# Kernel tuning notes

Measured on AMD Instinct MI355X. Metric: run time of the kernel, lower is better.

Reference implementation:

```python
import jax, jax.numpy as jnp
import numpy as np

SIDES, LAYERS, NH = 2, 2, 2
DEPTH, B = 7, 8
NPT = (3 ** DEPTH - 1) // 2  # 1093 nodes per perfect ternary tree
N = B * NPT                  # 8744
E, H = 256, 512
NUM_USERS, NUM_POIS, NUM_CATS, NUM_COOS, TMAX = 2000, 5000, 300, 50, 600
FUSE = NUM_POIS + NUM_CATS + NUM_COOS


def setup_inputs() -> dict:
    key = jax.random.key(0)
    cnt = [0]
    def nk():
        cnt[0] += 1
        return jax.random.fold_in(key, cnt[0])
    def rn(*s):
        return jax.random.normal(nk(), s, jnp.float32) * 0.02
    inp = dict(
        user_ids=jax.random.randint(nk(), (SIDES, N), 0, NUM_USERS, jnp.int32),
        feat_ids=jax.random.randint(nk(), (SIDES, N), 0, FUSE, jnp.int32),
        time_ids=jax.random.randint(nk(), (SIDES, N), 0, TMAX, jnp.int32),
        mask=jnp.ones((SIDES, N), jnp.int32),
        depth=DEPTH, n_trees=B,
        user_emb=rn(SIDES, NUM_USERS, 128), fuse_emb=rn(SIDES, FUSE, 128),
        time_pe=rn(SIDES, TMAX, E),
        Wf=rn(SIDES, H, E), bf=jnp.zeros((SIDES, H)),
        Wiou=rn(SIDES, 3 * H, E), Uiou=rn(SIDES, 3 * H, 3 * H), biou=jnp.zeros((SIDES, 3 * H)),
        attn_in_w=rn(SIDES, LAYERS, 3 * H, H), attn_in_b=jnp.zeros((SIDES, LAYERS, 3 * H)),
        attn_out_w=rn(SIDES, LAYERS, H, H), attn_out_b=jnp.zeros((SIDES, LAYERS, H)),
        ff1_w=rn(SIDES, LAYERS, H, H), ff1_b=jnp.zeros((SIDES, LAYERS, H)),
        ff2_w=rn(SIDES, LAYERS, H, H), ff2_b=jnp.zeros((SIDES, LAYERS, H)),
        ln1_w=jnp.ones((SIDES, LAYERS, H)), ln1_b=jnp.zeros((SIDES, LAYERS, H)),
        ln2_w=jnp.ones((SIDES, LAYERS, H)), ln2_b=jnp.zeros((SIDES, LAYERS, H)),
        dec_poi_w=rn(SIDES, NUM_POIS, H), dec_poi_b=jnp.zeros((SIDES, NUM_POIS)),
        dec_cat_w=rn(SIDES, NUM_CATS, H), dec_cat_b=jnp.zeros((SIDES, NUM_CATS)),
        dec_coo_w=rn(SIDES, NUM_COOS, H), dec_coo_b=jnp.zeros((SIDES, NUM_COOS)),
        cat2poi_w=rn(SIDES, NUM_POIS, NUM_CATS), cat2poi_b=jnp.zeros((SIDES, NUM_POIS)),
        coo2poi_w=rn(SIDES, NUM_POIS, NUM_COOS), coo2poi_b=jnp.zeros((SIDES, NUM_POIS)),
        mtl=jnp.ones((SIDES, 3)),
        c0=(jax.random.uniform(nk(), (SIDES, N, H), jnp.float32) * 2.0 - 1.0) * 0.025,
    )
    return inp


def _ln(x, w, b, eps=1e-5):
    m = x.mean(-1, keepdims=True)
    v = ((x - m) ** 2).mean(-1, keepdims=True)
    return (x - m) / jnp.sqrt(v + eps) * w + b


def _mha(x, iw, ib, ow, ob):
    M, S, Hd = x.shape
    q, k, v = jnp.split(x @ iw.T + ib, 3, -1)
    hd = Hd // NH
    def rs(t):
        return t.reshape(M, S, NH, hd).transpose(0, 2, 1, 3)
    q, k, v = rs(q), rs(k), rs(v)
    att = jax.nn.softmax((q * (hd ** -0.5)) @ k.transpose(0, 1, 3, 2), -1)
    o = (att @ v).transpose(0, 2, 1, 3).reshape(M, S, Hd)
    return o @ ow.T + ob


def _enc(x, iw, ib, ow, ob, f1w, f1b, f2w, f2b, l1w, l1b, l2w, l2b):
    # post-norm TransformerEncoderLayer, relu, eval mode (no dropout)
    x = _ln(x + _mha(x, iw, ib, ow, ob), l1w, l1b)
    return _ln(x + (jax.nn.relu(x @ f1w.T + f1b) @ f2w.T + f2b), l2w, l2b)


def _forward(user_ids, feat_ids, time_ids, mask, depth, n_trees,
             user_emb, fuse_emb, time_pe, Wf, bf, Wiou, Uiou, biou,
             attn_in_w, attn_in_b, attn_out_w, attn_out_b,
             ff1_w, ff1_b, ff2_w, ff2_b, ln1_w, ln1_b, ln2_w, ln2_b,
             dec_poi_w, dec_poi_b, dec_cat_w, dec_cat_b, dec_coo_w, dec_coo_b,
             cat2poi_w, cat2poi_b, coo2poi_w, coo2poi_b, mtl, c0):
    Hd = Wf.shape[1]
    npt = (3 ** depth - 1) // 2
    Bt = n_trees
    offs = [(3 ** l - 1) // 2 for l in range(depth)]
    outs = []
    for s in range(SIDES):
        m = mask[s]
        uid, fid, tid = user_ids[s] * m, feat_ids[s] * m, time_ids[s] * m
        emb = jnp.concatenate([user_emb[s][uid], fuse_emb[s][fid]], -1) + 0.5 * time_pe[s][tid]
        mf = m.astype(emb.dtype)[:, None]
        x = (emb * mf).reshape(Bt, npt, -1)              # masked node features
        iou0 = ((emb @ Wiou[s].T) * mf).reshape(Bt, npt, 3 * Hd)  # leaf iou init
        c0s = c0[s].reshape(Bt, npt, Hd)
        h = jnp.zeros((Bt, npt, Hd), emb.dtype)
        c = jnp.zeros((Bt, npt, Hd), emb.dtype)
        for l in range(depth - 1, -1, -1):  # bottom-up topo propagation, level-major layout
            st, n = offs[l], 3 ** l
            if l == depth - 1:  # leaves: no reduce, apply with initial iou and c
                iou = iou0[:, st:st + n]
                cpre = c0s[:, st:st + n]
            else:
                cs = offs[l + 1]
                hch = h[:, cs:cs + 3 * n].reshape(Bt * n, 3, Hd)   # mailbox h_child
                cch = c[:, cs:cs + 3 * n].reshape(Bt, n, 3, Hd)    # mailbox c_child
                z = hch
                for L in range(LAYERS):
                    z = _enc(z, attn_in_w[s, L], attn_in_b[s, L], attn_out_w[s, L], attn_out_b[s, L],
                             ff1_w[s, L], ff1_b[s, L], ff2_w[s, L], ff2_b[s, L],
                             ln1_w[s, L], ln1_b[s, L], ln2_w[s, L], ln2_b[s, L])
                hc = z.reshape(Bt, n, 3 * Hd)
                xl = x[:, st:st + n]
                Wx = xl @ Wf[s].T
                f = jax.nn.sigmoid(jnp.concatenate([Wx] * 3, -1) + hc + jnp.tile(bf[s], 3))
                iou = xl @ Wiou[s].T + hc @ Uiou[s].T + biou[s]
                cpre = jnp.sum(f.reshape(Bt, n, 3, Hd) * cch, axis=2)
            i, o, u = jnp.split(iou, 3, -1)
            cn = jax.nn.sigmoid(i) * jnp.tanh(u) + cpre
            hn = jax.nn.sigmoid(o) * jnp.tanh(cn)
            h = h.at[:, st:st + n].set(hn)
            c = c.at[:, st:st + n].set(cn)
        hN = h.reshape(-1, Hd)
        poi = hN @ dec_poi_w[s].T + dec_poi_b[s]
        cat = hN @ dec_cat_w[s].T + dec_cat_b[s]
        coo = hN @ dec_coo_w[s].T + dec_coo_b[s]
        p = mtl[s]
        poi_mt = (0.5 * jnp.exp(-p[0]) * poi + p[0]
                  + 0.5 * jnp.exp(-p[1]) * (cat @ cat2poi_w[s].T + cat2poi_b[s]) + p[1]
                  + 0.5 * jnp.exp(-p[2]) * (coo @ coo2poi_w[s].T + coo2poi_b[s]) + p[2])
        outs += [poi_mt, cat, coo]
    return tuple(outs)


def reference(user_ids, feat_ids, time_ids, mask, depth, n_trees,
              user_emb, fuse_emb, time_pe, Wf, bf, Wiou, Uiou, biou,
              attn_in_w, attn_in_b, attn_out_w, attn_out_b,
              ff1_w, ff1_b, ff2_w, ff2_b, ln1_w, ln1_b, ln2_w, ln2_b,
              dec_poi_w, dec_poi_b, dec_cat_w, dec_cat_b, dec_coo_w, dec_coo_b,
              cat2poi_w, cat2poi_b, coo2poi_w, coo2poi_b, mtl, c0):
    return _forward(user_ids, feat_ids, time_ids, mask, depth, n_trees,
                    user_emb, fuse_emb, time_pe, Wf, bf, Wiou, Uiou, biou,
                    attn_in_w, attn_in_b, attn_out_w, attn_out_b,
                    ff1_w, ff1_b, ff2_w, ff2_b, ln1_w, ln1_b, ln2_w, ln2_b,
                    dec_poi_w, dec_poi_b, dec_cat_w, dec_cat_b, dec_coo_w, dec_coo_b,
                    cat2poi_w, cat2poi_b, coo2poi_w, coo2poi_b, mtl, c0)
```

## Files before the change

kernel.cpp:

```cpp
#include <hip/hip_runtime.h>
#include <math.h>

#define SIDES 2
#define LAYERS 2
#define NTREE 8
#define NPT 1093
#define NN (NTREE*NPT)
#define EE 256
#define HH 512
#define NUSERS 2000
#define NPOI 5000
#define NCAT 300
#define NCOO 50
#define FUSEN 5350
#define TMAXN 600
#define TOKMAX 5832
#define PARMAX 1944

constexpr long OUT_S   = 46780400L;
constexpr long CAT_OFF = 43720000L;
constexpr long COO_OFF = 46343200L;

constexpr long H_S    = (long)NN*HH;
constexpr long X_S    = (long)NN*EE;
constexpr long Z_S    = (long)TOKMAX*HH;
constexpr long QKV_S  = (long)TOKMAX*3*HH;
constexpr long WXI_S  = (long)PARMAX*2048;
constexpr long WEFF_S = (long)NPOI*HH;

typedef __attribute__((ext_vector_type(8))) short  bf16x8;
typedef __attribute__((ext_vector_type(8))) ushort u16x8;
typedef __attribute__((ext_vector_type(4))) ushort u16x4;
typedef __attribute__((ext_vector_type(4))) float  f32x4;

__device__ __forceinline__ float sigm(float x){ return 1.f/(1.f+expf(-x)); }
__device__ __forceinline__ ushort f2b(float f){
  union { float f; unsigned u; } v; v.f = f;
  return (ushort)((v.u + 0x7fffu + ((v.u >> 16) & 1u)) >> 16);
}
__device__ __forceinline__ float b2f(ushort u){
  union { unsigned u; float f; } v; v.u = (unsigned)u << 16; return v.f;
}

constexpr int PB_EMB  = 2*NN;
constexpr int PB_MCVT = 6494;
constexpr int PB_WCOMB= 2*2048;
constexpr int PB_BCOMB= 16;
constexpr int PB_POI  = 2*5000;
constexpr int PB_TP   = 2*512;
constexpr int PB_WEI  = 2*2500;
constexpr int PB_BEF  = 40;
constexpr int PB_TOT  = PB_EMB+PB_MCVT+PB_WCOMB+PB_BCOMB+PB_POI+PB_TP+PB_WEI+PB_BEF;

__global__ void __launch_bounds__(256) prep_k(
    const int* __restrict__ uid, const int* __restrict__ fid,
    const int* __restrict__ tids, const int* __restrict__ mask,
    const float* __restrict__ uemb, const float* __restrict__ femb,
    const float* __restrict__ tpe, ushort* __restrict__ X,
    ushort* ainW, const float* attn_in_w, ushort* aoutW, const float* attn_out_w,
    ushort* f1W, const float* ff1_w, ushort* f2W, const float* ff2_w,
    ushort* dcatW, const float* dec_cat_w, ushort* dcooW, const float* dec_coo_w,
    ushort* wcomb, const float* Wf, const float* Wiou, const float* Uiou,
    float* bcomb, const float* biou,
    ushort* c2pB, const float* cat2poi_w, ushort* o2pB, const float* coo2poi_w,
    ushort* dcT2,
    ushort* weffB, const float* dec_poi_w, const float* mtl,
    float* beff, const float* dec_poi_b, const float* dec_cat_b,
    const float* cat2poi_b, const float* dec_coo_b, const float* coo2poi_b){
  int b = blockIdx.x;
  int tid = threadIdx.x;
  if (b < PB_EMB){
    int s = b / NN; long i = b - s*NN; int d = tid;
    int m = mask[(long)s*NN + i];
    int u = uid[(long)s*NN + i]*m, f = fid[(long)s*NN + i]*m, t = tids[(long)s*NN + i]*m;
    float e = (d < 128) ? uemb[((long)s*NUSERS + u)*128 + d]
                        : femb[((long)s*FUSEN + f)*128 + (d-128)];
    e += 0.5f * tpe[((long)s*TMAXN + t)*256 + d];
    X[(long)s*X_S + i*EE + d] = f2b(e * (float)m);
    return;
  }
  b -= PB_EMB;
  if (b < PB_MCVT){
    const long n0 = 3145728, n1 = 1048576, n2 = 1048576, n3 = 1048576,
               n4 = 307200, n5 = 51200;
    long i = ((long)b*256 + tid)*4;
    ushort* d; const float* s; long off;
    if      (i < n0){ d=ainW;  s=attn_in_w;  off=i; }
    else if ((i-=n0) < n1){ d=aoutW; s=attn_out_w; off=i; }
    else if ((i-=n1) < n2){ d=f1W;  s=ff1_w;  off=i; }
    else if ((i-=n2) < n3){ d=f2W;  s=ff2_w;  off=i; }
    else if ((i-=n3) < n4){ d=dcatW; s=dec_cat_w; off=i; }
    else if ((i-=n4) < n5){ d=dcooW; s=dec_coo_w; off=i; }
    else return;
    f32x4 v = *(const f32x4*)(s + off);
    *(u16x4*)(d + off) = (u16x4){f2b(v[0]), f2b(v[1]), f2b(v[2]), f2b(v[3])};
    return;
  }
  b -= PB_MCVT;
  if (b < PB_WCOMB){
    int s = b >> 11; int row = b & 2047;
    ushort* dst = wcomb + (long)s*2048*1792 + (long)row*1792;
    for (int col = tid; col < 1792; col += 256){
      float v;
      if (row < 512) v = (col < 256) ? Wf[((long)s*512 + row)*256 + col] : 0.f;
      else {
        int r = row - 512;
        v = (col < 256) ? Wiou[((long)s*1536 + r)*256 + col]
                        : Uiou[((long)s*1536 + r)*1536 + (col-256)];
      }
      dst[col] = f2b(v);
    }
    return;
  }
  b -= PB_WCOMB;
  if (b < PB_BCOMB){
    int s = b >> 3; int c = (b & 7)*256 + tid;
    bcomb[(long)s*2048 + c] = (c < 512) ? 0.f : biou[(long)s*1536 + (c-512)];
    return;
  }
  b -= PB_BCOMB;
  if (b < PB_POI){
    int s = b / 5000; int r = b - s*5000;
    float a1 = 0.5f*expf(-mtl[(long)s*3 + 1]);
    float a2 = 0.5f*expf(-mtl[(long)s*3 + 2]);
    for (int c = tid; c < 320; c += 256){
      float v = (c < 300) ? a1*cat2poi_w[((long)s*5000 + r)*300 + c] : 0.f;
      c2pB[((long)s*5000 + r)*320 + c] = f2b(v);
    }
    if (tid < 64){
      float v = (tid < 50) ? a2*coo2poi_w[((long)s*5000 + r)*50 + tid] : 0.f;
      o2pB[((long)s*5000 + r)*64 + tid] = f2b(v);
    }
    return;
  }
  b -= PB_POI;
  if (b < PB_TP){
    int s = b >> 9; int h = b & 511;
    ushort* dst = dcT2 + ((long)s*512 + h)*384;
    for (int c = tid; c < 384; c += 256){
      float v = 0.f;
      if (c < 300)                  v = dec_cat_w[((long)s*300 + c)*512 + h];
      else if (c >= 320 && c < 370) v = dec_coo_w[((long)s*50 + (c-320))*512 + h];
      dst[c] = f2b(v);
    }
    return;
  }
  b -= PB_TP;
  if (b < PB_WEI){
    int s = b / 2500; int blk = b - s*2500;
    long i = ((long)blk*256 + tid)*4;
    float a0 = 0.5f*expf(-mtl[(long)s*3]);
    f32x4 v = *(const f32x4*)(dec_poi_w + (long)s*WEFF_S + i);
    *(u16x4*)(weffB + (long)s*WEFF_S + i) =
        (u16x4){f2b(a0*v[0]), f2b(a0*v[1]), f2b(a0*v[2]), f2b(a0*v[3])};
    return;
  }
  b -= PB_WEI;
  {
    int s = b / 20; int n = (b - s*20)*256 + tid;
    if (n >= NPOI) return;
    const float* mt = mtl + (long)s*3;
    float a0 = 0.5f*expf(-mt[0]), a1 = 0.5f*expf(-mt[1]), a2 = 0.5f*expf(-mt[2]);
    float acc1 = 0.f, acc2 = 0.f;
    for (int c = 0; c < NCAT; c++)
      acc1 += dec_cat_b[(long)s*NCAT + c] * cat2poi_w[((long)s*NPOI + n)*NCAT + c];
    for (int c = 0; c < NCOO; c++)
      acc2 += dec_coo_b[(long)s*NCOO + c] * coo2poi_w[((long)s*NPOI + n)*NCOO + c];
    beff[(long)s*NPOI + n] = a0*dec_poi_b[(long)s*NPOI + n]
        + a1*(acc1 + cat2poi_b[(long)s*NPOI + n]) + a2*(acc2 + coo2poi_b[(long)s*NPOI + n])
        + mt[0] + mt[1] + mt[2];
  }
}

template<int MODE, bool OBF>
__global__ void __launch_bounds__(256)
mgemm_k(const ushort* __restrict__ A1, long lda1, long sA1,
        const ushort* __restrict__ A2, long lda2, long sA2,
        int kSplit, int mapN, int mapOff,
        const ushort* __restrict__ Wt, long ldw, long sW,
        const float* __restrict__ bias, long sB,
        void* __restrict__ Cv, long ldc, long sC,
        int M, int Nc, int K, int nbx,
        const float* __restrict__ mtl, int mtlIdx){
  int s = blockIdx.z;
  A1 += (long)s*sA1; A2 += (long)s*sA2; Wt += (long)s*sW;
  if (bias) bias += (long)s*sB;

  int flat = blockIdx.x, nwg = gridDim.x;
  int xcd = flat & 7, q = nwg >> 3, r8 = nwg & 7;
  int nf = (xcd < r8 ? xcd*(q+1) : r8*(q+1) + (xcd - r8)*q) + (flat >> 3);
  int bx = nf % nbx, by = nf / nbx;
  int m0 = by*128, n0 = bx*128;

  __shared__ ushort As[128*64];
  __shared__ ushort Ws[128*64];

  int tid = threadIdx.x;
  int lane = tid & 63, wave = tid >> 6;
  int wr = wave >> 1, wc = wave & 1;
  int fr = lane & 15, kc = lane >> 4;

  int baseRow = tid >> 3;
  int c16 = tid & 7;
  int col8 = c16*8;
  int swz = (baseRow & 7) << 4;

  long gA1[4], gA2[4], gW[4];
  int wbyte[4];
  #pragma unroll
  for (int c = 0; c < 4; c++){
    int row = baseRow + c*32;
    int ra = m0 + row; if (ra > M-1) ra = M-1;
    gA2[c] = ra;
    if (mapN > 0){ int tr = ra / mapN; gA1[c] = (long)(tr*NPT + mapOff + (ra - tr*mapN)); }
    else gA1[c] = ra;
    int rw = n0 + row; if (rw > Nc-1) rw = Nc-1;
    gW[c] = rw;
    wbyte[c] = row*128 + ((c16*16) ^ swz);
  }

  u16x8 rA[4], rW[4];
  {
    bool u1 = (0 < kSplit);
    const ushort* asrc = u1 ? A1 : A2;
    long ld = u1 ? lda1 : lda2;
    const long* g = u1 ? gA1 : gA2;
    #pragma unroll
    for (int c = 0; c < 4; c++){
      rA[c] = *(const u16x8*)(asrc + g[c]*ld + col8);
      rW[c] = *(const u16x8*)(Wt + gW[c]*ldw + col8);
    }
  }

  f32x4 acc[4][4];
  #pragma unroll
  for (int i = 0; i < 4; i++)
    #pragma unroll
    for (int j = 0; j < 4; j++) acc[i][j] = (f32x4){0.f,0.f,0.f,0.f};

  for (int k0 = 0; k0 < K; k0 += 64){
    #pragma unroll
    for (int c = 0; c < 4; c++){
      *(u16x8*)((char*)As + wbyte[c]) = rA[c];
      *(u16x8*)((char*)Ws + wbyte[c]) = rW[c];
    }
    __syncthreads();
    int kn = k0 + 64;
    if (kn < K){
      bool u1 = (kn < kSplit);
      const ushort* asrc = u1 ? A1 : A2;
      long ld = u1 ? lda1 : lda2;
      const long* g = u1 ? gA1 : gA2;
      long colb = u1 ? (long)kn : (long)(kn - kSplit);
      #pragma unroll
      for (int c = 0; c < 4; c++){
        rA[c] = *(const u16x8*)(asrc + g[c]*ld + colb + col8);
        rW[c] = *(const u16x8*)(Wt + gW[c]*ldw + kn + col8);
      }
    }
    #pragma unroll
    for (int h = 0; h < 2; h++){
      bf16x8 af[4], bw[4];
      #pragma unroll
      for (int i = 0; i < 4; i++){
        int row = wr*64 + i*16 + fr;
        int byo = row*128 + ((h*64 + kc*16) ^ ((row & 7) << 4));
        af[i] = *(const bf16x8*)((const char*)As + byo);
      }
      #pragma unroll
      for (int j = 0; j < 4; j++){
        int row = wc*64 + j*16 + fr;
        int byo = row*128 + ((h*64 + kc*16) ^ ((row & 7) << 4));
        bw[j] = *(const bf16x8*)((const char*)Ws + byo);
      }
      #pragma unroll
      for (int i = 0; i < 4; i++)
        #pragma unroll
        for (int j = 0; j < 4; j++)
          acc[i][j] = __builtin_amdgcn_mfma_f32_16x16x32_bf16(bw[j], af[i], acc[i][j], 0, 0, 0);
    }
    __syncthreads();
  }

  float alpha = 1.f;
  if (MODE == 4) alpha = 0.5f*expf(-mtl[(long)s*3 + mtlIdx]);
  int ccol = lane & 15, cr4 = (lane >> 4)*4;
  bool vecN = ((Nc & 3) == 0);
  float* Cf = (float*)Cv + (long)s*sC;
  ushort* Cb = (ushort*)Cv + (long)s*sC;
  #pragma unroll
  for (int i = 0; i < 4; i++){
    int gm = m0 + wr*64 + i*16 + ccol;
    if (gm >= M) continue;
    long rowoff = (long)gm*ldc;
    #pragma unroll
    for (int j = 0; j < 4; j++){
      int gn0 = n0 + wc*64 + j*16 + cr4;
      if (gn0 >= Nc) continue;
      f32x4 v = acc[i][j];
      if (MODE != 4 && MODE != 2 && bias){ f32x4 bv = *(const f32x4*)&bias[gn0]; v += bv; }
      if (MODE == 1){ v = (f32x4){fmaxf(v[0],0.f),fmaxf(v[1],0.f),fmaxf(v[2],0.f),fmaxf(v[3],0.f)}; }
      if (OBF){
        u16x4* cp = (u16x4*)&Cb[rowoff + gn0];
        if (MODE == 4 || MODE == 2){
          u16x4 o = *cp;
          float a = (MODE == 4) ? alpha : 1.f;
          *cp = (u16x4){f2b(b2f(o[0]) + a*v[0]), f2b(b2f(o[1]) + a*v[1]),
                        f2b(b2f(o[2]) + a*v[2]), f2b(b2f(o[3]) + a*v[3])};
        } else {
          *cp = (u16x4){f2b(v[0]), f2b(v[1]), f2b(v[2]), f2b(v[3])};
        }
      } else {
        if (vecN){
          f32x4* cp = (f32x4*)&Cf[rowoff + gn0];
          if (MODE == 4){ f32x4 o = *cp; *cp = o + alpha*v; }
          else if (MODE == 2){ f32x4 o = *cp; *cp = o + v; }
          else *cp = v;
        } else {
          #pragma unroll
          for (int r = 0; r < 4; r++){
            int gn = gn0 + r; if (gn >= Nc) continue;
            if (MODE == 4) Cf[rowoff + gn] += alpha*v[r];
            else if (MODE == 2) Cf[rowoff + gn] += v[r];
            else Cf[rowoff + gn] = v[r];
          }
        }
      }
    }
  }
}

__global__ void __launch_bounds__(256) attn_k(const ushort* __restrict__ qkv,
                                              ushort* __restrict__ o){
  int s = blockIdx.z;
  int w = threadIdx.x >> 6, lane = threadIdx.x & 63;
  int seq = blockIdx.x*2 + (w >> 1);
  int h = w & 1;
  const ushort* base = qkv + (long)s*QKV_S + (long)seq*3*1536 + h*256 + lane*4;
  float q[3][4], k[3][4], v[3][4];
  #pragma unroll
  for (int i = 0; i < 3; i++){
    u16x4 tq = *(const u16x4*)(base + (long)i*1536);
    u16x4 tk = *(const u16x4*)(base + (long)i*1536 + 512);
    u16x4 tv = *(const u16x4*)(base + (long)i*1536 + 1024);
    #pragma unroll
    for (int e = 0; e < 4; e++){ q[i][e]=b2f(tq[e]); k[i][e]=b2f(tk[e]); v[i][e]=b2f(tv[e]); }
  }
  float p[9];
  #pragma unroll
  for (int i = 0; i < 3; i++)
    #pragma unroll
    for (int j = 0; j < 3; j++){
      float acc = 0.f;
      #pragma unroll
      for (int e = 0; e < 4; e++) acc += q[i][e]*k[j][e];
      p[i*3+j] = acc;
    }
  #pragma unroll
  for (int m = 1; m < 64; m <<= 1)
    #pragma unroll
    for (int t = 0; t < 9; t++) p[t] += __shfl_xor(p[t], m);
  float att[9];
  #pragma unroll
  for (int i = 0; i < 3; i++){
    float a = p[i*3]*0.0625f, bb = p[i*3+1]*0.0625f, c = p[i*3+2]*0.0625f;
    float mx = fmaxf(a, fmaxf(bb, c));
    a = expf(a-mx); bb = expf(bb-mx); c = expf(c-mx);
    float inv = 1.f/(a+bb+c);
    att[i*3] = a*inv; att[i*3+1] = bb*inv; att[i*3+2] = c*inv;
  }
  ushort* ob = o + (long)s*Z_S + (long)seq*1536 + h*256 + lane*4;
  #pragma unroll
  for (int i = 0; i < 3; i++){
    u16x4 r;
    #pragma unroll
    for (int e = 0; e < 4; e++)
      r[e] = f2b(att[i*3]*v[0][e] + att[i*3+1]*v[1][e] + att[i*3+2]*v[2][e]);
    *(u16x4*)(ob + (long)i*512) = r;
  }
}

__global__ void __launch_bounds__(256) add_ln_k(ushort* __restrict__ zout, long sZ,
                         const ushort* __restrict__ res, long sR, int mapN, int mapOff,
                         const ushort* __restrict__ tb, long sT,
                         const float* __restrict__ w, const float* __restrict__ b,
                         long wstr){
  int s = blockIdx.z;
  int wv = threadIdx.x >> 6, lane = threadIdx.x & 63;
  int r = blockIdx.x*4 + wv;
  int g = r;
  if (mapN > 0){ int tr = r / mapN; g = tr*NPT + mapOff + (r - tr*mapN); }
  int d0 = lane*8;
  u16x8 rr = *(const u16x8*)(res + (long)s*sR + (long)g*HH + d0);
  u16x8 tt = *(const u16x8*)(tb  + (long)s*sT + (long)r*HH + d0);
  float x[8];
  float sum = 0.f;
  #pragma unroll
  for (int e = 0; e < 8; e++){ x[e] = b2f(rr[e]) + b2f(tt[e]); sum += x[e]; }
  #pragma unroll
  for (int m = 1; m < 64; m <<= 1) sum += __shfl_xor(sum, m);
  float mean = sum * (1.f/512.f);
  float vs = 0.f;
  #pragma unroll
  for (int e = 0; e < 8; e++){ float d = x[e]-mean; vs += d*d; }
  #pragma unroll
  for (int m = 1; m < 64; m <<= 1) vs += __shfl_xor(vs, m);
  float inv = 1.f/sqrtf(vs*(1.f/512.f) + 1e-5f);
  const float* wr_ = w + (long)s*wstr + d0;
  const float* br_ = b + (long)s*wstr + d0;
  f32x4 w0 = *(const f32x4*)wr_, w1 = *(const f32x4*)(wr_+4);
  f32x4 b0 = *(const f32x4*)br_, b1 = *(const f32x4*)(br_+4);
  u16x8 ov;
  #pragma unroll
  for (int e = 0; e < 4; e++){
    ov[e]   = f2b((x[e]-mean)*inv*w0[e] + b0[e]);
    ov[e+4] = f2b((x[e+4]-mean)*inv*w1[e] + b1[e]);
  }
  *(u16x8*)(zout + (long)s*sZ + (long)r*HH + d0) = ov;
}

__global__ void leaf_k(const ushort* __restrict__ iou, const float* __restrict__ c0,
                       ushort* __restrict__ hbuf, float* __restrict__ cbuf){
  int s = blockIdx.z, p = blockIdx.x;
  int tree = p / 729, j = p - tree*729;
  long row = (long)(tree*NPT + 364 + j)*HH;
  const ushort* iour = iou + (long)s*QKV_S + (long)p*1536;
  const float* c0r = c0 + (long)s*H_S + row;
  for (int d = threadIdx.x; d < HH; d += 256){
    float cn = sigm(b2f(iour[d])) * tanhf(b2f(iour[1024 + d])) + c0r[d];
    float hn = sigm(b2f(iour[512 + d])) * tanhf(cn);
    hbuf[(long)s*H_S + row + d] = f2b(hn);
    cbuf[(long)s*H_S + row + d] = cn;
  }
}

__global__ void combine_k(const ushort* __restrict__ wxiou, const ushort* __restrict__ z,
                          const float* __restrict__ bfv, const float* __restrict__ cbuf,
                          ushort* __restrict__ hbuf, float* __restrict__ cout,
                          int n, int st, int cs){
  int s = blockIdx.z, p = blockIdx.x;
  int tree = p / n, j = p - tree*n;
  const ushort* wr_ = wxiou + (long)s*WXI_S + (long)p*2048;
  const ushort* zr  = z + (long)s*Z_S + (long)p*1536;
  const float* bfr  = bfv + (long)s*HH;
  const float* cch  = cbuf + (long)s*H_S + (long)(tree*NPT + cs + 3*j)*HH;
  long orow = (long)s*H_S + (long)(tree*NPT + st + j)*HH;
  for (int d = threadIdx.x; d < HH; d += 256){
    float wv = b2f(wr_[d]) + bfr[d];
    float cpre = 0.f;
    #pragma unroll
    for (int ch = 0; ch < 3; ch++){
      float fg = sigm(wv + b2f(zr[ch*512 + d]));
      cpre += fg * cch[ch*512 + d];
    }
    float iv = b2f(wr_[512 + d]), ov = b2f(wr_[1024 + d]), uv = b2f(wr_[1536 + d]);
    float cn = sigm(iv)*tanhf(uv) + cpre;
    float hn = sigm(ov)*tanhf(cn);
    hbuf[orow + d] = f2b(hn);
    cout[orow + d] = cn;
  }
}

#define GEMM(MODE, OBF, A1, LDA1, SA1, A2, LDA2, SA2, KSPL, MAPN, MAPOFF, WT, LDW, SW, \
             BI, SB, CC, LDC, SC, M, NC, K)                                            \
  do { int nbx_ = ((NC)+127)/128, nby_ = ((M)+127)/128;                                \
    mgemm_k<MODE, OBF><<<dim3(nbx_*nby_, 1, SIDES), 256, 0, stream>>>(                 \
      A1, LDA1, SA1, A2, LDA2, SA2, KSPL, MAPN, MAPOFF, WT, LDW, SW, BI, SB,           \
      CC, LDC, SC, M, NC, K, nbx_, mtl, 0); } while(0)

extern "C" void kernel_launch(void* const* d_in, const int* in_sizes, int n_in,
                              void* d_out, int out_size, void* d_ws, size_t ws_size,
                              hipStream_t stream){
  (void)in_sizes; (void)n_in; (void)out_size; (void)ws_size;
  const int*   user_ids  = (const int*)d_in[0];
  const int*   feat_ids  = (const int*)d_in[1];
  const int*   time_ids  = (const int*)d_in[2];
  const int*   mask      = (const int*)d_in[3];
  const float* user_emb  = (const float*)d_in[6];
  const float* fuse_emb  = (const float*)d_in[7];
  const float* time_pe   = (const float*)d_in[8];
  const float* Wf        = (const float*)d_in[9];
  const float* bf        = (const float*)d_in[10];
  const float* Wiou      = (const float*)d_in[11];
  const float* Uiou      = (const float*)d_in[12];
  const float* biou      = (const float*)d_in[13];
  const float* attn_in_w = (const float*)d_in[14];
  const float* attn_in_b = (const float*)d_in[15];
  const float* attn_out_w= (const float*)d_in[16];
  const float* attn_out_b= (const float*)d_in[17];
  const float* ff1_w     = (const float*)d_in[18];
  const float* ff1_b     = (const float*)d_in[19];
  const float* ff2_w     = (const float*)d_in[20];
  const float* ff2_b     = (const float*)d_in[21];
  const float* ln1_w     = (const float*)d_in[22];
  const float* ln1_b     = (const float*)d_in[23];
  const float* ln2_w     = (const float*)d_in[24];
  const float* ln2_b     = (const float*)d_in[25];
  const float* dec_poi_w = (const float*)d_in[26];
  const float* dec_poi_b = (const float*)d_in[27];
  const float* dec_cat_w = (const float*)d_in[28];
  const float* dec_cat_b = (const float*)d_in[29];
  const float* dec_coo_w = (const float*)d_in[30];
  const float* dec_coo_b = (const float*)d_in[31];
  const float* cat2poi_w = (const float*)d_in[32];
  const float* cat2poi_b = (const float*)d_in[33];
  const float* coo2poi_w = (const float*)d_in[34];
  const float* coo2poi_b = (const float*)d_in[35];
  const float* mtl       = (const float*)d_in[36];
  const float* c0        = (const float*)d_in[37];

  float* out = (float*)d_out;

  ushort* wsu = (ushort*)d_ws;
  ushort* Hb    = wsu;
  ushort* ainW  = Hb    + 2*H_S;
  ushort* aoutW = ainW  + (long)2*2*1536*512;
  ushort* f1W   = aoutW + (long)2*2*512*512;
  ushort* f2W   = f1W   + (long)2*2*512*512;
  ushort* wcomb = f2W   + (long)2*2*512*512;
  ushort* dcatW = wcomb + (long)2*2048*1792;
  ushort* dcooW = dcatW + (long)2*300*512;
  ushort* weffB = dcooW + (long)2*50*512;
  float*  bcomb = (float*)(weffB + (long)2*WEFF_S);
  float*  beff  = bcomb + 2*2048;

  float*  Cb   = out + OUT_S;
  ushort* osu  = (ushort*)(Cb + 2*H_S);
  ushort* QKV  = osu;
  ushort* Zb   = QKV  + 2*QKV_S;
  ushort* TMP  = Zb   + 2*Z_S;
  ushort* WXI  = TMP  + 2*Z_S;
  ushort* Xb   = WXI  + 2*WXI_S;
  ushort* c2pB = Xb   + 2*X_S;
  ushort* o2pB = c2pB + (long)2*5000*320;
  ushort* dcT2 = o2pB + (long)2*5000*64;

  prep_k<<<dim3(PB_TOT), 256, 0, stream>>>(
      user_ids, feat_ids, time_ids, mask, user_emb, fuse_emb, time_pe, Xb,
      ainW, attn_in_w, aoutW, attn_out_w, f1W, ff1_w, f2W, ff2_w,
      dcatW, dec_cat_w, dcooW, dec_coo_w,
      wcomb, Wf, Wiou, Uiou, bcomb, biou,
      c2pB, cat2poi_w, o2pB, coo2poi_w, dcT2,
      weffB, dec_poi_w, mtl,
      beff, dec_poi_b, dec_cat_b, cat2poi_b, dec_coo_b, coo2poi_b);

  GEMM(0, true, Xb, 256L, X_S, Xb, 256L, X_S, 256, 729, 364,
       wcomb + (long)512*1792, 1792L, (long)2048*1792,
       (const float*)nullptr, 0L, QKV, 1536L, QKV_S, 5832, 1536, 256);
  leaf_k<<<dim3(5832, 1, SIDES), 256, 0, stream>>>(QKV, c0, Hb, Cb);

  const int p3[7]   = {1,3,9,27,81,243,729};
  const int offs[7] = {0,1,4,13,40,121,364};

  for (int l = 5; l >= 0; l--){
    int n = p3[l], st = offs[l], cs = offs[l+1];
    int P = NTREE*n, T = 3*P;
    for (int L = 0; L < LAYERS; L++){
      const ushort* zin = (L == 0) ? Hb : Zb;
      long zs = (L == 0) ? H_S : Z_S;
      int mN = (L == 0) ? 3*n : 0, mO = (L == 0) ? cs : 0;
      GEMM(0, true, zin, 512L, zs, zin, 512L, zs, 512, mN, mO,
           ainW + (long)L*1536*512, 512L, (long)2*1536*512,
           attn_in_b + (long)L*1536, (long)LAYERS*1536, QKV, 1536L, QKV_S, T, 1536, 512);
      attn_k<<<dim3(P/2, 1, SIDES), 256, 0, stream>>>(QKV, TMP);
      GEMM(0, true, TMP, 512L, Z_S, TMP, 512L, Z_S, 512, 0, 0,
           aoutW + (long)L*512*512, 512L, (long)2*512*512,
           attn_out_b + (long)L*512, (long)LAYERS*512, QKV, 512L, QKV_S, T, 512, 512);
      add_ln_k<<<dim3(T/4, 1, SIDES), 256, 0, stream>>>(Zb, Z_S, zin, zs, mN, mO,
           QKV, QKV_S, ln1_w + (long)L*512, ln1_b + (long)L*512, (long)LAYERS*512);
      GEMM(1, true, Zb, 512L, Z_S, Zb, 512L, Z_S, 512, 0, 0,
           f1W + (long)L*512*512, 512L, (long)2*512*512,
           ff1_b + (long)L*512, (long)LAYERS*512, TMP, 512L, Z_S, T, 512, 512);
      GEMM(0, true, TMP, 512L, Z_S, TMP, 512L, Z_S, 512, 0, 0,
           f2W + (long)L*512*512, 512L, (long)2*512*512,
           ff2_b + (long)L*512, (long)LAYERS*512, QKV, 512L, QKV_S, T, 512, 512);
      add_ln_k<<<dim3(T/4, 1, SIDES), 256, 0, stream>>>(Zb, Z_S, Zb, Z_S, 0, 0,
           QKV, QKV_S, ln2_w + (long)L*512, ln2_b + (long)L*512, (long)LAYERS*512);
    }
    GEMM(0, true, Xb, 256L, X_S, Zb, 1536L, Z_S, 256, n, st,
         wcomb, 1792L, (long)2048*1792, bcomb, 2048L, WXI, 2048L, WXI_S, P, 2048, 1792);
    combine_k<<<dim3(P, 1, SIDES), 256, 0, stream>>>(WXI, Zb, bf, Cb, Hb, Cb, n, st, cs);
  }

  GEMM(0, false, Hb, 512L, H_S, Hb, 512L, H_S, 512, 0, 0,
       dcatW, 512L, (long)NCAT*512, dec_cat_b, (long)NCAT,
       out + CAT_OFF, (long)NCAT, OUT_S, NN, NCAT, 512);
  GEMM(0, false, Hb, 512L, H_S, Hb, 512L, H_S, 512, 0, 0,
       dcooW, 512L, (long)NCOO*512, dec_coo_b, (long)NCOO,
       out + COO_OFF, (long)NCOO, OUT_S, NN, NCOO, 512);

  GEMM(2, true, c2pB, 320L, (long)5000*320, o2pB, 64L, (long)5000*64, 320, 0, 0,
       dcT2, 384L, (long)512*384, (const float*)nullptr, 0L,
       weffB, 512L, WEFF_S, 5000, 512, 384);

  GEMM(0, false, Hb, 512L, H_S, Hb, 512L, H_S, 512, 0, 0,
       weffB, 512L, WEFF_S, beff, (long)NPOI,
       out, (long)NPOI, OUT_S, NN, NPOI, 512);
}
```

Baseline: 1.554 ms.

## Fuse 3-token attention into the attention-output GEMM prologue

Removes the standalone attention kernel. Each GEMM block now computes the QK scores and softmax for its row range into shared memory, then builds the attention output on the fly while staging the A tile from the V columns. This drops one launch and the write and read of the intermediate attention buffer. In exchange, each of the 4 column blocks recomputes the scores, every A-tile load now reads three V rows with fp32 math in the load path, and the output goes to TMP instead of QKV.

```diff
diff --git a/kernel.cpp b/kernel.cpp
--- a/kernel.cpp
+++ b/kernel.cpp
@@ -172,7 +172,7 @@
   }
 }
 
-template<int MODE, bool OBF>
+template<int MODE, bool OBF, bool FATTN>
 __global__ void __launch_bounds__(256)
 mgemm_k(const ushort* __restrict__ A1, long lda1, long sA1,
         const ushort* __restrict__ A2, long lda2, long sA2,
@@ -194,6 +194,7 @@
 
   __shared__ ushort As[128*64];
   __shared__ ushort Ws[128*64];
+  __shared__ float satt[FATTN ? 792 : 1];
 
   int tid = threadIdx.x;
   int lane = tid & 63, wave = tid >> 6;
@@ -219,16 +220,76 @@
     wbyte[c] = row*128 + ((c16*16) ^ swz);
   }
 
+  int s0q = 0;
+  if constexpr (FATTN){
+    s0q = m0/3;
+    int lastRow = m0 + 127; if (lastRow > M-1) lastRow = M-1;
+    int nseq = lastRow/3 - s0q + 1;
+    for (int task = tid; task < nseq*18; task += 256){
+      int sl = task/18, rem = task - sl*18;
+      int h = rem/9, ij = rem - h*9;
+      int i2 = ij/3, j2 = ij - i2*3;
+      const ushort* qp = A1 + ((long)((s0q+sl)*3 + i2))*lda1 + h*256;
+      const ushort* kp = A1 + ((long)((s0q+sl)*3 + j2))*lda1 + 512 + h*256;
+      float accd = 0.f;
+      for (int c = 0; c < 256; c += 8){
+        u16x8 qv = *(const u16x8*)(qp + c);
+        u16x8 kv = *(const u16x8*)(kp + c);
+        #pragma unroll
+        for (int e = 0; e < 8; e++) accd += b2f(qv[e])*b2f(kv[e]);
+      }
+      satt[task] = accd * 0.0625f;
+    }
+    __syncthreads();
+    for (int task = tid; task < nseq*6; task += 256){
+      int sl = task/6, rem = task - sl*6;
+      int h = rem/3, i2 = rem - h*3;
+      float* p = &satt[sl*18 + h*9 + i2*3];
+      float a = p[0], bq = p[1], cq = p[2];
+      float mx = fmaxf(a, fmaxf(bq, cq));
+      a = expf(a-mx); bq = expf(bq-mx); cq = expf(cq-mx);
+      float inv = 1.f/(a+bq+cq);
+      p[0] = a*inv; p[1] = bq*inv; p[2] = cq*inv;
+    }
+    __syncthreads();
+  }
+
+  auto stageA = [&](int c, long kb) -> u16x8 {
+    int ra = (int)gA1[c];
+    int seq = ra/3, tok = ra - seq*3, sl = seq - s0q;
+    long d = kb + col8;
+    int h = (int)(d >> 8);
+    const float* at = &satt[sl*18 + h*9 + tok*3];
+    const ushort* vb = A1 + ((long)seq*3)*lda1 + 1024 + d;
+    u16x8 v0 = *(const u16x8*)(vb);
+    u16x8 v1 = *(const u16x8*)(vb + lda1);
+    u16x8 v2 = *(const u16x8*)(vb + 2*lda1);
+    float a0 = at[0], a1 = at[1], a2 = at[2];
+    u16x8 r;
+    #pragma unroll
+    for (int e = 0; e < 8; e++)
+      r[e] = f2b(a0*b2f(v0[e]) + a1*b2f(v1[e]) + a2*b2f(v2[e]));
+    return r;
+  };
+
   u16x8 rA[4], rW[4];
   {
-    bool u1 = (0 < kSplit);
-    const ushort* asrc = u1 ? A1 : A2;
-    long ld = u1 ? lda1 : lda2;
-    const long* g = u1 ? gA1 : gA2;
-    #pragma unroll
-    for (int c = 0; c < 4; c++){
-      rA[c] = *(const u16x8*)(asrc + g[c]*ld + col8);
-      rW[c] = *(const u16x8*)(Wt + gW[c]*ldw + col8);
+    if constexpr (FATTN){
+      #pragma unroll
+      for (int c = 0; c < 4; c++){
+        rA[c] = stageA(c, 0);
+        rW[c] = *(const u16x8*)(Wt + gW[c]*ldw + col8);
+      }
+    } else {
+      bool u1 = (0 < kSplit);
+      const ushort* asrc = u1 ? A1 : A2;
+      long ld = u1 ? lda1 : lda2;
+      const long* g = u1 ? gA1 : gA2;
+      #pragma unroll
+      for (int c = 0; c < 4; c++){
+        rA[c] = *(const u16x8*)(asrc + g[c]*ld + col8);
+        rW[c] = *(const u16x8*)(Wt + gW[c]*ldw + col8);
+      }
     }
   }
 
@@ -247,15 +308,23 @@
     __syncthreads();
     int kn = k0 + 64;
     if (kn < K){
-      bool u1 = (kn < kSplit);
-      const ushort* asrc = u1 ? A1 : A2;
-      long ld = u1 ? lda1 : lda2;
-      const long* g = u1 ? gA1 : gA2;
-      long colb = u1 ? (long)kn : (long)(kn - kSplit);
-      #pragma unroll
-      for (int c = 0; c < 4; c++){
-        rA[c] = *(const u16x8*)(asrc + g[c]*ld + colb + col8);
-        rW[c] = *(const u16x8*)(Wt + gW[c]*ldw + kn + col8);
+      if constexpr (FATTN){
+        #pragma unroll
+        for (int c = 0; c < 4; c++){
+          rA[c] = stageA(c, kn);
+          rW[c] = *(const u16x8*)(Wt + gW[c]*ldw + kn + col8);
+        }
+      } else {
+        bool u1 = (kn < kSplit);
+        const ushort* asrc = u1 ? A1 : A2;
+        long ld = u1 ? lda1 : lda2;
+        const long* g = u1 ? gA1 : gA2;
+        long colb = u1 ? (long)kn : (long)(kn - kSplit);
+        #pragma unroll
+        for (int c = 0; c < 4; c++){
+          rA[c] = *(const u16x8*)(asrc + g[c]*ld + colb + col8);
+          rW[c] = *(const u16x8*)(Wt + gW[c]*ldw + kn + col8);
+        }
       }
     }
     #pragma unroll
@@ -330,56 +399,6 @@
   }
 }
 
-__global__ void __launch_bounds__(256) attn_k(const ushort* __restrict__ qkv,
-                                              ushort* __restrict__ o){
-  int s = blockIdx.z;
-  int w = threadIdx.x >> 6, lane = threadIdx.x & 63;
-  int seq = blockIdx.x*2 + (w >> 1);
-  int h = w & 1;
-  const ushort* base = qkv + (long)s*QKV_S + (long)seq*3*1536 + h*256 + lane*4;
-  float q[3][4], k[3][4], v[3][4];
-  #pragma unroll
-  for (int i = 0; i < 3; i++){
-    u16x4 tq = *(const u16x4*)(base + (long)i*1536);
-    u16x4 tk = *(const u16x4*)(base + (long)i*1536 + 512);
-    u16x4 tv = *(const u16x4*)(base + (long)i*1536 + 1024);
-    #pragma unroll
-    for (int e = 0; e < 4; e++){ q[i][e]=b2f(tq[e]); k[i][e]=b2f(tk[e]); v[i][e]=b2f(tv[e]); }
-  }
-  float p[9];
-  #pragma unroll
-  for (int i = 0; i < 3; i++)
-    #pragma unroll
-    for (int j = 0; j < 3; j++){
-      float acc = 0.f;
-      #pragma unroll
-      for (int e = 0; e < 4; e++) acc += q[i][e]*k[j][e];
-      p[i*3+j] = acc;
-    }
-  #pragma unroll
-  for (int m = 1; m < 64; m <<= 1)
-    #pragma unroll
-    for (int t = 0; t < 9; t++) p[t] += __shfl_xor(p[t], m);
-  float att[9];
-  #pragma unroll
-  for (int i = 0; i < 3; i++){
-    float a = p[i*3]*0.0625f, bb = p[i*3+1]*0.0625f, c = p[i*3+2]*0.0625f;
-    float mx = fmaxf(a, fmaxf(bb, c));
-    a = expf(a-mx); bb = expf(bb-mx); c = expf(c-mx);
-    float inv = 1.f/(a+bb+c);
-    att[i*3] = a*inv; att[i*3+1] = bb*inv; att[i*3+2] = c*inv;
-  }
-  ushort* ob = o + (long)s*Z_S + (long)seq*1536 + h*256 + lane*4;
-  #pragma unroll
-  for (int i = 0; i < 3; i++){
-    u16x4 r;
-    #pragma unroll
-    for (int e = 0; e < 4; e++)
-      r[e] = f2b(att[i*3]*v[0][e] + att[i*3+1]*v[1][e] + att[i*3+2]*v[2][e]);
-    *(u16x4*)(ob + (long)i*512) = r;
-  }
-}
-
 __global__ void __launch_bounds__(256) add_ln_k(ushort* __restrict__ zout, long sZ,
                          const ushort* __restrict__ res, long sR, int mapN, int mapOff,
                          const ushort* __restrict__ tb, long sT,
@@ -464,9 +483,14 @@
 #define GEMM(MODE, OBF, A1, LDA1, SA1, A2, LDA2, SA2, KSPL, MAPN, MAPOFF, WT, LDW, SW, \
              BI, SB, CC, LDC, SC, M, NC, K)                                            \
   do { int nbx_ = ((NC)+127)/128, nby_ = ((M)+127)/128;                                \
-    mgemm_k<MODE, OBF><<<dim3(nbx_*nby_, 1, SIDES), 256, 0, stream>>>(                 \
+    mgemm_k<MODE, OBF, false><<<dim3(nbx_*nby_, 1, SIDES), 256, 0, stream>>>(          \
       A1, LDA1, SA1, A2, LDA2, SA2, KSPL, MAPN, MAPOFF, WT, LDW, SW, BI, SB,           \
       CC, LDC, SC, M, NC, K, nbx_, mtl, 0); } while(0)
+#define GEMMFA(QKVP, WT, LDW, SW, BI, SB, CC, LDC, SC, M)                              \
+  do { int nbx_ = 4, nby_ = ((M)+127)/128;                                            \
+    mgemm_k<0, true, true><<<dim3(nbx_*nby_, 1, SIDES), 256, 0, stream>>>(             \
+      QKVP, 1536L, QKV_S, QKVP, 1536L, QKV_S, 512, 0, 0, WT, LDW, SW, BI, SB,          \
+      CC, LDC, SC, M, 512, 512, nbx_, mtl, 0); } while(0)
 
 extern "C" void kernel_launch(void* const* d_in, const int* in_sizes, int n_in,
                               void* d_out, int out_size, void* d_ws, size_t ws_size,
@@ -562,12 +586,10 @@
       GEMM(0, true, zin, 512L, zs, zin, 512L, zs, 512, mN, mO,
            ainW + (long)L*1536*512, 512L, (long)2*1536*512,
            attn_in_b + (long)L*1536, (long)LAYERS*1536, QKV, 1536L, QKV_S, T, 1536, 512);
-      attn_k<<<dim3(P/2, 1, SIDES), 256, 0, stream>>>(QKV, TMP);
-      GEMM(0, true, TMP, 512L, Z_S, TMP, 512L, Z_S, 512, 0, 0,
-           aoutW + (long)L*512*512, 512L, (long)2*512*512,
-           attn_out_b + (long)L*512, (long)LAYERS*512, QKV, 512L, QKV_S, T, 512, 512);
+      GEMMFA(QKV, aoutW + (long)L*512*512, 512L, (long)2*512*512,
+             attn_out_b + (long)L*512, (long)LAYERS*512, TMP, 512L, Z_S, T);
       add_ln_k<<<dim3(T/4, 1, SIDES), 256, 0, stream>>>(Zb, Z_S, zin, zs, mN, mO,
-           QKV, QKV_S, ln1_w + (long)L*512, ln1_b + (long)L*512, (long)LAYERS*512);
+           TMP, Z_S, ln1_w + (long)L*512, ln1_b + (long)L*512, (long)LAYERS*512);
       GEMM(1, true, Zb, 512L, Z_S, Zb, 512L, Z_S, 512, 0, 0,
            f1W + (long)L*512*512, 512L, (long)2*512*512,
            ff1_b + (long)L*512, (long)LAYERS*512, TMP, 512L, Z_S, T, 512, 512);
```

After: 1.777 ms. +14.3%, slower.

## Widen GEMM tile to 128x256 with each wave owning a 64-column strip

Applied to the files above, without the earlier changes.

The GEMM block tile grows from 128x128 to 128x256 along N. The wave layout changes so each of the four waves covers all 128 rows and its own 64-column slice, which doubles the accumulators per wave to 8x4 MFMA tiles. The aim is more reuse of the A tile and fewer blocks, at the cost of more registers, twice the W shared memory, and fewer blocks for small-N GEMMs. A launch bound of 2 blocks per CU is added to limit register growth.

```diff
diff --git a/kernel.cpp b/kernel.cpp
--- a/kernel.cpp
+++ b/kernel.cpp
@@ -173,7 +173,7 @@
 }
 
 template<int MODE, bool OBF>
-__global__ void __launch_bounds__(256)
+__global__ void __launch_bounds__(256, 2)
 mgemm_k(const ushort* __restrict__ A1, long lda1, long sA1,
         const ushort* __restrict__ A2, long lda2, long sA2,
         int kSplit, int mapN, int mapOff,
@@ -190,23 +190,21 @@
   int xcd = flat & 7, q = nwg >> 3, r8 = nwg & 7;
   int nf = (xcd < r8 ? xcd*(q+1) : r8*(q+1) + (xcd - r8)*q) + (flat >> 3);
   int bx = nf % nbx, by = nf / nbx;
-  int m0 = by*128, n0 = bx*128;
+  int m0 = by*128, n0 = bx*256;
 
   __shared__ ushort As[128*64];
-  __shared__ ushort Ws[128*64];
+  __shared__ ushort Ws[256*64];
 
   int tid = threadIdx.x;
   int lane = tid & 63, wave = tid >> 6;
-  int wr = wave >> 1, wc = wave & 1;
   int fr = lane & 15, kc = lane >> 4;
 
   int baseRow = tid >> 3;
   int c16 = tid & 7;
   int col8 = c16*8;
-  int swz = (baseRow & 7) << 4;
-
-  long gA1[4], gA2[4], gW[4];
-  int wbyte[4];
+
+  long gA1[4], gA2[4], gW[8];
+  int abyte[4], wbyte[8];
   #pragma unroll
   for (int c = 0; c < 4; c++){
     int row = baseRow + c*32;
@@ -214,36 +212,43 @@
     gA2[c] = ra;
     if (mapN > 0){ int tr = ra / mapN; gA1[c] = (long)(tr*NPT + mapOff + (ra - tr*mapN)); }
     else gA1[c] = ra;
+    abyte[c] = row*128 + ((c16*16) ^ ((row & 7) << 4));
+  }
+  #pragma unroll
+  for (int c = 0; c < 8; c++){
+    int row = baseRow + c*32;
     int rw = n0 + row; if (rw > Nc-1) rw = Nc-1;
     gW[c] = rw;
-    wbyte[c] = row*128 + ((c16*16) ^ swz);
-  }
-
-  u16x8 rA[4], rW[4];
+    wbyte[c] = row*128 + ((c16*16) ^ ((row & 7) << 4));
+  }
+
+  u16x8 rA[4], rW[8];
   {
     bool u1 = (0 < kSplit);
     const ushort* asrc = u1 ? A1 : A2;
     long ld = u1 ? lda1 : lda2;
     const long* g = u1 ? gA1 : gA2;
     #pragma unroll
-    for (int c = 0; c < 4; c++){
+    for (int c = 0; c < 4; c++)
       rA[c] = *(const u16x8*)(asrc + g[c]*ld + col8);
+    #pragma unroll
+    for (int c = 0; c < 8; c++)
       rW[c] = *(const u16x8*)(Wt + gW[c]*ldw + col8);
-    }
-  }
-
-  f32x4 acc[4][4];
-  #pragma unroll
-  for (int i = 0; i < 4; i++)
+  }
+
+  f32x4 acc[8][4];
+  #pragma unroll
+  for (int i = 0; i < 8; i++)
     #pragma unroll
     for (int j = 0; j < 4; j++) acc[i][j] = (f32x4){0.f,0.f,0.f,0.f};
 
   for (int k0 = 0; k0 < K; k0 += 64){
     #pragma unroll
-    for (int c = 0; c < 4; c++){
-      *(u16x8*)((char*)As + wbyte[c]) = rA[c];
+    for (int c = 0; c < 4; c++)
+      *(u16x8*)((char*)As + abyte[c]) = rA[c];
+    #pragma unroll
+    for (int c = 0; c < 8; c++)
       *(u16x8*)((char*)Ws + wbyte[c]) = rW[c];
-    }
     __syncthreads();
     int kn = k0 + 64;
     if (kn < K){
@@ -251,33 +256,32 @@
       const ushort* asrc = u1 ? A1 : A2;
       long ld = u1 ? lda1 : lda2;
       const long* g = u1 ? gA1 : gA2;
-      long colb = u1 ? (long)kn : (long)(kn - kSplit);
+      long colb = (u1 ? (long)kn : (long)(kn - kSplit)) + col8;
       #pragma unroll
-      for (int c = 0; c < 4; c++){
-        rA[c] = *(const u16x8*)(asrc + g[c]*ld + colb + col8);
+      for (int c = 0; c < 4; c++)
+        rA[c] = *(const u16x8*)(asrc + g[c]*ld + colb);
+      #pragma unroll
+      for (int c = 0; c < 8; c++)
         rW[c] = *(const u16x8*)(Wt + gW[c]*ldw + kn + col8);
-      }
     }
     #pragma unroll
     for (int h = 0; h < 2; h++){
-      bf16x8 af[4], bw[4];
-      #pragma unroll
-      for (int i = 0; i < 4; i++){
-        int row = wr*64 + i*16 + fr;
-        int byo = row*128 + ((h*64 + kc*16) ^ ((row & 7) << 4));
-        af[i] = *(const bf16x8*)((const char*)As + byo);
-      }
+      bf16x8 bw[4];
       #pragma unroll
       for (int j = 0; j < 4; j++){
-        int row = wc*64 + j*16 + fr;
+        int row = wave*64 + j*16 + fr;
         int byo = row*128 + ((h*64 + kc*16) ^ ((row & 7) << 4));
         bw[j] = *(const bf16x8*)((const char*)Ws + byo);
       }
       #pragma unroll
-      for (int i = 0; i < 4; i++)
+      for (int i = 0; i < 8; i++){
+        int row = i*16 + fr;
+        int byo = row*128 + ((h*64 + kc*16) ^ ((row & 7) << 4));
+        bf16x8 af = *(const bf16x8*)((const char*)As + byo);
         #pragma unroll
         for (int j = 0; j < 4; j++)
-          acc[i][j] = __builtin_amdgcn_mfma_f32_16x16x32_bf16(bw[j], af[i], acc[i][j], 0, 0, 0);
+          acc[i][j] = __builtin_amdgcn_mfma_f32_16x16x32_bf16(bw[j], af, acc[i][j], 0, 0, 0);
+      }
     }
     __syncthreads();
   }
@@ -289,13 +293,13 @@
   float* Cf = (float*)Cv + (long)s*sC;
   ushort* Cb = (ushort*)Cv + (long)s*sC;
   #pragma unroll
-  for (int i = 0; i < 4; i++){
-    int gm = m0 + wr*64 + i*16 + ccol;
+  for (int i = 0; i < 8; i++){
+    int gm = m0 + i*16 + ccol;
     if (gm >= M) continue;
     long rowoff = (long)gm*ldc;
     #pragma unroll
     for (int j = 0; j < 4; j++){
-      int gn0 = n0 + wc*64 + j*16 + cr4;
+      int gn0 = n0 + wave*64 + j*16 + cr4;
       if (gn0 >= Nc) continue;
       f32x4 v = acc[i][j];
       if (MODE != 4 && MODE != 2 && bias){ f32x4 bv = *(const f32x4*)&bias[gn0]; v += bv; }
@@ -463,7 +467,7 @@
 
 #define GEMM(MODE, OBF, A1, LDA1, SA1, A2, LDA2, SA2, KSPL, MAPN, MAPOFF, WT, LDW, SW, \
              BI, SB, CC, LDC, SC, M, NC, K)                                            \
-  do { int nbx_ = ((NC)+127)/128, nby_ = ((M)+127)/128;                                \
+  do { int nbx_ = ((NC)+255)/256, nby_ = ((M)+127)/128;                                \
     mgemm_k<MODE, OBF><<<dim3(nbx_*nby_, 1, SIDES), 256, 0, stream>>>(                 \
       A1, LDA1, SA1, A2, LDA2, SA2, KSPL, MAPN, MAPOFF, WT, LDW, SW, BI, SB,           \
       CC, LDC, SC, M, NC, K, nbx_, mtl, 0); } while(0)
```

Result: slower. 2.019 ms (+29.9%).
